# Performance work log

Measured on AMD Instinct MI355X. Metric: run time of the kernel, lower is better.

Reference implementation:

```python
import jax, jax.numpy as jnp
import numpy as np

B, C, H, W = 2, 32, 128, 128
K = 5            # window_size
NH = 2           # num_heads
HD = C // NH     # head_dim = 16
KK = K * K
HID = int(2 * C * 2.0)  # mlp hidden = dim*2*mlp_ratio = 128
SCALE = HD ** -0.5


def _ln(x, w, b, eps=1e-5):
    m = jnp.mean(x, -1, keepdims=True)
    v = jnp.var(x, -1, keepdims=True)
    return (x - m) * jax.lax.rsqrt(v + eps) * w + b


def _windows(t):
    # t: [B,H,W,C] -> [B,H,W,C,K*K]; zero-padded KxK neighborhood per pixel
    # (same layout as nn.Unfold: kernel position is the fastest-varying axis).
    p = (K - 1) // 2
    Hc, Wc = t.shape[1], t.shape[2]
    tp = jnp.pad(t, ((0, 0), (p, p), (p, p), (0, 0)))
    return jnp.stack([tp[:, i:i + Hc, j:j + Wc, :] for i in range(K) for j in range(K)], axis=-1)


def _rel_index():
    # Swin-style relative position index for a KxK window -> [KK,KK] ints
    c = jnp.stack(jnp.meshgrid(jnp.arange(K), jnp.arange(K), indexing='ij'), 0).reshape(2, -1)
    r = (c[:, :, None] - c[:, None, :]).transpose(1, 2, 0) + (K - 1)
    return r[..., 0] * (2 * K - 1) + r[..., 1]


def _ckbd_mask(h, w):
    # checkerboard attention mask: [L, KK, KK] additive (0 or -100)
    ck = jnp.zeros((h, w), jnp.float32)
    ck = ck.at[0::2, 1::2].set(1.0).at[1::2, 0::2].set(1.0)
    cw = _windows(ck[None, :, :, None])[0, :, :, 0, :].reshape(h * w, KK)  # [L,KK]
    m = cw[:, :, None] * cw[:, None, :]
    return jnp.where(m == 1.0, 0.0, -100.0)


def setup_inputs() -> dict:
    key = jax.random.key(0)
    ks = jax.random.split(key, 8)
    p = lambda k, s: (0.02 * jax.random.normal(k, s)).astype(jnp.float32)
    return dict(
        x=jax.random.normal(ks[0], (B, C, H, W), dtype=jnp.float32),
        qkv_w=p(ks[1], (3 * C, C)), qkv_b=jnp.zeros((3 * C,), jnp.float32),
        rel_table=p(ks[2], ((2 * K - 1) ** 2, NH)),
        norm1_w=jnp.ones((C,), jnp.float32), norm1_b=jnp.zeros((C,), jnp.float32),
        norm2_w=jnp.ones((2 * C,), jnp.float32), norm2_b=jnp.zeros((2 * C,), jnp.float32),
        proj_w=p(ks[3], (2 * C, 2 * C)), proj_b=jnp.zeros((2 * C,), jnp.float32),
        fusion_w=p(ks[4], (2 * C, C, K, K)), fusion_b=jnp.zeros((2 * C,), jnp.float32),
        mlp_w1=p(ks[5], (HID, 2 * C)), mlp_b1=jnp.zeros((HID,), jnp.float32),
        mlp_w2=p(ks[6], (2 * C, HID)), mlp_b2=jnp.zeros((2 * C,), jnp.float32),
    )


def reference(x, qkv_w, qkv_b, rel_table, norm1_w, norm1_b, norm2_w, norm2_b,
              proj_w, proj_b, fusion_w, fusion_b, mlp_w1, mlp_b1, mlp_w2, mlp_b2):
    Bs, Cs, Hs, Ws = x.shape
    L = Hs * Ws
    xt = x.reshape(Bs, Cs, L).transpose(0, 2, 1)          # [B,L,C]
    xn = _ln(xt, norm1_w, norm1_b)
    qkv = jnp.einsum('blc,oc->blo', xn, qkv_w) + qkv_b     # [B,L,3C]
    qkv = qkv.reshape(Bs, Hs, Ws, 3, Cs)
    q, k, v = qkv[..., 0, :], qkv[..., 1, :], qkv[..., 2, :]  # each [B,H,W,C]

    def heads(t):
        # windows -> [B,L,C,KK]; split C as (head_dim, num_heads) to match the
        # original reshape(B,L,head_dim,num_heads,KK).permute(0,1,3,4,2)
        w_ = _windows(t).reshape(Bs, L, HD, NH, KK)
        return w_.transpose(0, 1, 3, 4, 2)                 # [B,L,nh,KK,hd]

    qh, kh, vh = heads(q), heads(k), heads(v)
    attn = jnp.einsum('blhqd,blhkd->blhqk', qh * SCALE, kh)  # [B,L,nh,KK,KK]

    bias = rel_table[_rel_index().reshape(-1)].reshape(KK, KK, NH).transpose(2, 0, 1)
    attn = attn + bias[None, None]
    attn = attn + _ckbd_mask(Hs, Ws)[None, :, None]
    attn = jax.nn.softmax(attn, axis=-1)

    o = jnp.einsum('blhqk,blhkd->blhqd', attn, vh)           # [B,L,nh,KK,hd]
    # -> [B,L,K,K,nh,hd] -> [B,L,K,K,C] (head-major channel order, as in torch)
    o = o.reshape(Bs, L, NH, K, K, HD).transpose(0, 1, 3, 4, 2, 5).reshape(Bs, L, K, K, Cs)
    # fusion: Conv2d(C, 2C, kernel=K) on [BL,C,K,K] with no padding == full contraction
    y = jnp.einsum('blijc,ocij->blo', o, fusion_w) + fusion_b  # [B,L,2C]
    y = jnp.einsum('blc,oc->blo', y, proj_w) + proj_b
    h1 = _ln(y, norm2_w, norm2_b)
    mlp = jnp.einsum('blh,oh->blo',
                     jax.nn.gelu(jnp.einsum('blc,hc->blh', h1, mlp_w1) + mlp_b1, approximate=False),
                     mlp_w2) + mlp_b2
    y = y + mlp
    return y.transpose(0, 2, 1).reshape(Bs, 2 * Cs, Hs, Ws)
```

## Files before the change

### kernel.cpp

```cpp
#include <hip/hip_runtime.h>
#include <cstdint>
#include <cstddef>

#define HH 128
#define WW 128
#define LL 16384
#define BL 32768

typedef float  f32x4  __attribute__((ext_vector_type(4)));
typedef __fp16 h2     __attribute__((ext_vector_type(2)));
typedef __fp16 h8     __attribute__((ext_vector_type(8)));

union U32H { unsigned u; h2 h; };

static __device__ __forceinline__ float fdot2(h2 a, h2 b, float c) {
  return __builtin_amdgcn_fdot2(a, b, c, false);
}
static __device__ __forceinline__ unsigned pkh2(float a, float b) {
  h2 h = __builtin_amdgcn_cvt_pkrtz(a, b);
  U32H t; t.h = h; return t.u;
}
static __device__ __forceinline__ h2 bcasth(float a) {
  return __builtin_amdgcn_cvt_pkrtz(a, a);
}
static __device__ __forceinline__ unsigned short f2h(float x) {
  union { __fp16 h; unsigned short u; } c; c.h = (__fp16)x; return c.u;
}

#define LOADH8(dst, ptr) { \
  uint4 _a = *(const uint4*)(ptr); uint4 _b = *(const uint4*)((ptr)+8); U32H _t; \
  _t.u=_a.x; dst[0]=_t.h; _t.u=_a.y; dst[1]=_t.h; _t.u=_a.z; dst[2]=_t.h; _t.u=_a.w; dst[3]=_t.h; \
  _t.u=_b.x; dst[4]=_t.h; _t.u=_b.y; dst[5]=_t.h; _t.u=_b.z; dst[6]=_t.h; _t.u=_b.w; dst[7]=_t.h; }

__global__ __launch_bounds__(256) void k_combine(
    const float* __restrict__ proj_w, const float* __restrict__ proj_b,
    const float* __restrict__ fw, const float* __restrict__ fb,
    const float* __restrict__ w1, const float* __restrict__ w2,
    unsigned short* __restrict__ wctT, float* __restrict__ bc,
    unsigned short* __restrict__ w1h, unsigned short* __restrict__ w2h)
{
  if (blockIdx.x == 200) {
    int o = threadIdx.x;
    if (o < 64) {
      float acc = proj_b[o];
      for (int m = 0; m < 64; ++m) acc = fmaf(proj_w[o*64+m], fb[m], acc);
      bc[o] = acc;
    }
    return;
  }
  if (blockIdx.x == 201) {
    for (int i = threadIdx.x; i < 8192; i += 256) w1h[i] = f2h(w1[i]);
    return;
  }
  if (blockIdx.x == 202) {
    for (int i = threadIdx.x; i < 8192; i += 256) w2h[i] = f2h(w2[i]);
    return;
  }
  int gid = blockIdx.x * 256 + threadIdx.x;
  int o  = gid / 800;
  int kk = gid - o * 800;
  int c  = kk & 31;
  int t  = kk >> 5;
  int in = c * 25 + t;
  float acc = 0.f;
  for (int m = 0; m < 64; ++m) acc = fmaf(proj_w[o*64+m], fw[m*800+in], acc);
  wctT[gid] = f2h(acc);
}

__global__ __launch_bounds__(128) void k_ln_qkv(
    const float* __restrict__ x, const float* __restrict__ qkv_w,
    const float* __restrict__ qkv_b, const float* __restrict__ n1w,
    const float* __restrict__ n1b, unsigned short* __restrict__ qo,
    unsigned short* __restrict__ ko, unsigned short* __restrict__ vo)
{
  __shared__ float sW[32*32];
  __shared__ float sB[32];
  __shared__ float sNw[32], sNb[32];
  int p = blockIdx.y;
  for (int i = threadIdx.x; i < 32*32; i += 128) sW[i] = qkv_w[p*1024 + i];
  if (threadIdx.x < 32) {
    sB[threadIdx.x]  = qkv_b[p*32 + threadIdx.x];
    sNw[threadIdx.x] = n1w[threadIdx.x];
    sNb[threadIdx.x] = n1b[threadIdx.x];
  }
  __syncthreads();
  int gid = blockIdx.x * 128 + threadIdx.x;
  int b = gid >> 14, l = gid & (LL - 1);
  const float* xp = x + (size_t)b * 32 * LL + l;
  float xv[32];
  float mean = 0.f;
  #pragma unroll
  for (int c = 0; c < 32; ++c) { xv[c] = xp[(size_t)c * LL]; mean += xv[c]; }
  mean *= 0.03125f;
  float var = 0.f;
  #pragma unroll
  for (int c = 0; c < 32; ++c) { float d = xv[c] - mean; var = fmaf(d, d, var); }
  float rs = rsqrtf(var * 0.03125f + 1e-5f);
  #pragma unroll
  for (int c = 0; c < 32; ++c) xv[c] = (xv[c] - mean) * rs * sNw[c] + sNb[c];
  float ao[32];
  #pragma unroll
  for (int o = 0; o < 32; ++o) {
    const float* wr = &sW[o * 32];
    float acc = sB[o];
    #pragma unroll
    for (int c = 0; c < 32; ++c) acc = fmaf(xv[c], wr[c], acc);
    ao[(o & 1) * 16 + (o >> 1)] = acc;
  }
  unsigned short* op = (p == 0 ? qo : p == 1 ? ko : vo) + (size_t)gid * 32;
  #pragma unroll
  for (int e = 0; e < 4; ++e) {
    uint4 pk4;
    pk4.x = pkh2(ao[e*8+0], ao[e*8+1]);
    pk4.y = pkh2(ao[e*8+2], ao[e*8+3]);
    pk4.z = pkh2(ao[e*8+4], ao[e*8+5]);
    pk4.w = pkh2(ao[e*8+6], ao[e*8+7]);
    *(uint4*)(op + e*8) = pk4;
  }
}

#define TH 4
#define TW 8
#define NPOS 96
#define KVSTR 24
#define OSTRU 264

__global__ __launch_bounds__(256, 3) void k_attn(
    const unsigned short* __restrict__ qi, const unsigned short* __restrict__ ki,
    const unsigned short* __restrict__ vi, const float* __restrict__ rel_table,
    const unsigned short* __restrict__ wctT, const float* __restrict__ bc,
    float* __restrict__ y2)
{
  __shared__ __align__(16) unsigned short sQ[192*KVSTR];
  __shared__ __align__(16) unsigned short sK[192*KVSTR];
  __shared__ __align__(16) unsigned short sV[192*KVSTR];
  __shared__ __align__(16) unsigned short sO[32*OSTRU];
  __shared__ float sRT[162];
  __shared__ float sPar[NPOS];

  int tid = threadIdx.x;
  int lane = tid & 63, wv = tid >> 6;
  int b  = blockIdx.z;
  int h0 = blockIdx.y * TH, w0 = blockIdx.x * TW;

  for (int i = tid; i < 162; i += 256) sRT[i] = rel_table[i];
  if (tid < NPOS) {
    int ph = tid / 12, pw = tid - ph * 12;
    int h2v = h0 + ph - 2, w2v = w0 + pw - 2;
    bool valid = ((unsigned)h2v < HH) && ((unsigned)w2v < WW);
    sPar[tid] = (valid && (((h2v + w2v) & 1) == 1)) ? 1.f : 0.f;
  }
  for (int idx = tid; idx < 1152; idx += 256) {
    int arr = idx / 384;
    int rem = idx - arr * 384;
    int pos = rem >> 2, q4 = rem & 3;
    int nh = q4 >> 1, half = q4 & 1;
    int ph = pos / 12, pw = pos - ph * 12;
    int h2v = h0 + ph - 2, w2v = w0 + pw - 2;
    uint4 val = make_uint4(0u, 0u, 0u, 0u);
    if (((unsigned)h2v < HH) && ((unsigned)w2v < WW)) {
      const unsigned short* src = (arr == 0 ? ki : arr == 1 ? vi : qi)
                       + ((size_t)((b << 14) + (h2v << 7) + w2v)) * 32 + nh * 16 + half * 8;
      val = *(const uint4*)src;
    }
    unsigned short* dp = (arr == 0 ? sK : arr == 1 ? sV : sQ)
                       + (nh * 96 + pos) * KVSTR + half * 8;
    *(uint4*)dp = val;
  }
  __syncthreads();

  f32x4 acc[2] = {{0.f,0.f,0.f,0.f},{0.f,0.f,0.f,0.f}};
  int ocol = wv * 16 + (lane & 15);

  for (int it = 0; it < 4; ++it) {
    int g = wv * 2 + (lane >> 5);
    int pr = it * 4 + (g >> 1);
    int nh = g & 1;
    int nhb = nh * 96;
    if (pr <= 12) {
      int nrr = (pr < 12) ? 2 : 1;
      int loc = lane & 31;
      int ly = loc >> 3, lx = loc & 7;
      int posb = ly * 12 + lx;
      int tq0 = 2*pr, tq1 = 2*pr + 1;
      int iq0 = tq0/5, jq0 = tq0 - iq0*5;
      int iq1 = tq1/5, jq1 = tq1 - iq1*5;
      int pq0 = posb + iq0*12 + jq0; pq0 = pq0 > 95 ? 95 : pq0;
      int pq1 = posb + iq1*12 + jq1; pq1 = pq1 > 95 ? 95 : pq1;
      float parq0 = sPar[pq0], parq1 = sPar[pq1];
      h2 q0[8], q1[8];
      LOADH8(q0, &sQ[(nhb+pq0)*KVSTR]);
      LOADH8(q1, &sQ[(nhb+pq1)*KVSTR]);
      float s0 = 0.f, s1 = 0.f;
      h2 oo0[8], oo1[8];
      #pragma unroll
      for (int e = 0; e < 8; ++e) { oo0[e] = (h2)(__fp16)0.f; oo1[e] = (h2)(__fp16)0.f; }
      #pragma unroll 1
      for (int ik = 0; ik < 5; ++ik) {
        int rb0 = ((iq0-ik+4)*9 + jq0 + 4)*2 + nh;
        int rb1 = ((iq1-ik+4)*9 + jq1 + 4)*2 + nh;
        #pragma unroll
        for (int jk = 0; jk < 5; ++jk) {
          int pk = posb + ik*12 + jk;
          h2 kh[8];
          LOADH8(kh, &sK[(nhb+pk)*KVSTR]);
          float park = sPar[pk];
          float mk = (park == 1.f) ? 0.f : -100.f;
          float a0 = 0.f, a1 = 0.f;
          #pragma unroll
          for (int u = 0; u < 8; ++u) {
            a0 = fdot2(q0[u], kh[u], a0);
            a1 = fdot2(q1[u], kh[u], a1);
          }
          int i0 = rb0 - 2*jk; i0 = i0 > 161 ? 161 : i0;
          int i1 = rb1 - 2*jk; i1 = i1 > 161 ? 161 : i1;
          float e0 = __expf(fmaf(parq0, mk, fmaf(a0, 0.25f, sRT[i0])));
          float e1 = __expf(fmaf(parq1, mk, fmaf(a1, 0.25f, sRT[i1])));
          s0 += e0; s1 += e1;
          h2 e0h = bcasth(e0), e1h = bcasth(e1);
          h2 vh[8];
          LOADH8(vh, &sV[(nhb+pk)*KVSTR]);
          #pragma unroll
          for (int u = 0; u < 8; ++u) {
            oo0[u] = e0h * vh[u] + oo0[u];
            oo1[u] = e1h * vh[u] + oo1[u];
          }
        }
      }
      #define WRITE_ROW(OO, SS, TQ) { \
        h2 ih = bcasth(1.f / (SS)); \
        int kl = ((TQ) - it*8) * 32 + nh * 16; \
        union { h2 h[8]; uint4 u4[2]; } R; \
        _Pragma("unroll") \
        for (int u = 0; u < 8; ++u) R.h[u] = OO[u] * ih; \
        *(uint4*)&sO[loc*OSTRU + kl] = R.u4[0]; \
        *(uint4*)&sO[loc*OSTRU + kl + 8] = R.u4[1]; }
      WRITE_ROW(oo0, s0, tq0);
      if (1 < nrr) WRITE_ROW(oo1, s1, tq1);
      #undef WRITE_ROW
    }
    __syncthreads();
    int ktn = (it < 3) ? 8 : 1;
    const unsigned short* bcol = wctT + (size_t)ocol * 800 + it * 256 + (lane >> 4) * 8;
    for (int kt = 0; kt < ktn; ++kt) {
      h8 bfrag = *(const h8*)(bcol + kt * 32);
      #pragma unroll
      for (int mt = 0; mt < 2; ++mt) {
        h8 afrag = *(const h8*)&sO[(mt*16 + (lane & 15))*OSTRU + kt*32 + (lane >> 4)*8];
        acc[mt] = __builtin_amdgcn_mfma_f32_16x16x32_f16(afrag, bfrag, acc[mt], 0, 0, 0);
      }
    }
    __syncthreads();
  }
  float bco = bc[ocol];
  #pragma unroll
  for (int mt = 0; mt < 2; ++mt) {
    #pragma unroll
    for (int r2 = 0; r2 < 4; ++r2) {
      int loc = mt * 16 + (lane >> 4) * 4 + r2;
      int ly = loc >> 3, lx = loc & 7;
      int gid = (b << 14) + ((h0 + ly) << 7) + (w0 + lx);
      y2[(size_t)gid * 64 + ocol] = acc[mt][r2] + bco;
    }
  }
}

__global__ __launch_bounds__(256) void k_mlp(
    const float* __restrict__ y2, const float* __restrict__ n2w,
    const float* __restrict__ n2b, const unsigned short* __restrict__ w1h,
    const float* __restrict__ b1, const unsigned short* __restrict__ w2h,
    const float* __restrict__ b2, float* __restrict__ out)
{
  __shared__ __align__(16) unsigned short sA[64*72];
  __shared__ __align__(16) unsigned short sH[64*136];
  int tid = threadIdx.x;
  int lane = tid & 63, wv = tid >> 6;
  int m0 = blockIdx.x * 64;
  {
    int r = tid >> 2, qd = tid & 3;
    const float* yp = y2 + (size_t)(m0 + r) * 64 + qd * 16;
    float xv[16];
    float s = 0.f;
    #pragma unroll
    for (int e = 0; e < 4; ++e) {
      float4 t4 = *(const float4*)(yp + e*4);
      xv[4*e] = t4.x; xv[4*e+1] = t4.y; xv[4*e+2] = t4.z; xv[4*e+3] = t4.w;
      s += t4.x + t4.y + t4.z + t4.w;
    }
    s += __shfl_xor(s, 1);
    s += __shfl_xor(s, 2);
    float mean = s * (1.f/64.f);
    float v = 0.f;
    #pragma unroll
    for (int e = 0; e < 16; ++e) { float d = xv[e] - mean; v = fmaf(d, d, v); }
    v += __shfl_xor(v, 1);
    v += __shfl_xor(v, 2);
    float rs = rsqrtf(v * (1.f/64.f) + 1e-5f);
    #pragma unroll
    for (int u = 0; u < 8; ++u) {
      int c0 = qd*16 + 2*u;
      float h0v = (xv[2*u]   - mean) * rs * n2w[c0]   + n2b[c0];
      float h1v = (xv[2*u+1] - mean) * rs * n2w[c0+1] + n2b[c0+1];
      *(unsigned*)&sA[r*72 + c0] = pkh2(h0v, h1v);
    }
  }
  __syncthreads();
  f32x4 acc1[4][2];
  #pragma unroll
  for (int mt = 0; mt < 4; ++mt)
    #pragma unroll
    for (int nt = 0; nt < 2; ++nt) acc1[mt][nt] = (f32x4){0.f,0.f,0.f,0.f};
  #pragma unroll
  for (int kt = 0; kt < 2; ++kt) {
    #pragma unroll
    for (int nt = 0; nt < 2; ++nt) {
      int ncol = wv*32 + nt*16 + (lane & 15);
      h8 bfrag = *(const h8*)(w1h + ncol*64 + kt*32 + (lane >> 4)*8);
      #pragma unroll
      for (int mt = 0; mt < 4; ++mt) {
        h8 afrag = *(const h8*)&sA[(mt*16 + (lane & 15))*72 + kt*32 + (lane >> 4)*8];
        acc1[mt][nt] = __builtin_amdgcn_mfma_f32_16x16x32_f16(afrag, bfrag, acc1[mt][nt], 0, 0, 0);
      }
    }
  }
  #pragma unroll
  for (int nt = 0; nt < 2; ++nt) {
    int ncol = wv*32 + nt*16 + (lane & 15);
    float b1v = b1[ncol];
    #pragma unroll
    for (int mt = 0; mt < 4; ++mt) {
      #pragma unroll
      for (int r2 = 0; r2 < 4; ++r2) {
        int mrow = mt*16 + (lane >> 4)*4 + r2;
        float h = acc1[mt][nt][r2] + b1v;
        float g = 0.5f * h * (1.f + erff(h * 0.70710678118f));
        sH[mrow*136 + ncol] = f2h(g);
      }
    }
  }
  __syncthreads();
  f32x4 acc2[4];
  #pragma unroll
  for (int mt = 0; mt < 4; ++mt) acc2[mt] = (f32x4){0.f,0.f,0.f,0.f};
  int ocol = wv*16 + (lane & 15);
  #pragma unroll
  for (int kt = 0; kt < 4; ++kt) {
    h8 bfrag = *(const h8*)(w2h + ocol*128 + kt*32 + (lane >> 4)*8);
    #pragma unroll
    for (int mt = 0; mt < 4; ++mt) {
      h8 afrag = *(const h8*)&sH[(mt*16 + (lane & 15))*136 + kt*32 + (lane >> 4)*8];
      acc2[mt] = __builtin_amdgcn_mfma_f32_16x16x32_f16(afrag, bfrag, acc2[mt], 0, 0, 0);
    }
  }
  float b2v = b2[ocol];
  int bb = m0 >> 14;
  #pragma unroll
  for (int mt = 0; mt < 4; ++mt) {
    int mrow = mt*16 + (lane >> 4)*4;
    int l = m0 + mrow;
    const float* yp = y2 + (size_t)l * 64 + ocol;
    float4 o4;
    o4.x = yp[0]   + acc2[mt][0] + b2v;
    o4.y = yp[64]  + acc2[mt][1] + b2v;
    o4.z = yp[128] + acc2[mt][2] + b2v;
    o4.w = yp[192] + acc2[mt][3] + b2v;
    *(float4*)&out[(size_t)bb * 64 * LL + (size_t)ocol * LL + (l - (bb << 14))] = o4;
  }
}

extern "C" void kernel_launch(void* const* d_in, const int* in_sizes, int n_in,
                              void* d_out, int out_size, void* d_ws, size_t ws_size,
                              hipStream_t stream) {
  const float* x         = (const float*)d_in[0];
  const float* qkv_w     = (const float*)d_in[1];
  const float* qkv_b     = (const float*)d_in[2];
  const float* rel_table = (const float*)d_in[3];
  const float* n1w       = (const float*)d_in[4];
  const float* n1b       = (const float*)d_in[5];
  const float* n2w       = (const float*)d_in[6];
  const float* n2b       = (const float*)d_in[7];
  const float* proj_w    = (const float*)d_in[8];
  const float* proj_b    = (const float*)d_in[9];
  const float* fw        = (const float*)d_in[10];
  const float* fb        = (const float*)d_in[11];
  const float* w1        = (const float*)d_in[12];
  const float* b1        = (const float*)d_in[13];
  const float* w2        = (const float*)d_in[14];
  const float* b2        = (const float*)d_in[15];

  char* ws = (char*)d_ws;
  unsigned short* q    = (unsigned short*)(ws);
  unsigned short* k    = (unsigned short*)(ws + 2097152);
  unsigned short* v    = (unsigned short*)(ws + 4194304);
  float*          y2   = (float*)(ws + 6291456);
  unsigned short* wctT = (unsigned short*)(ws + 14680064);
  float*          bc   = (float*)(ws + 14782464);
  unsigned short* w1h  = (unsigned short*)(ws + 14782720);
  unsigned short* w2h  = (unsigned short*)(ws + 14799104);
  float* out = (float*)d_out;

  k_combine<<<203, 256, 0, stream>>>(proj_w, proj_b, fw, fb, w1, w2, wctT, bc, w1h, w2h);
  k_ln_qkv<<<dim3(BL/128, 3), 128, 0, stream>>>(x, qkv_w, qkv_b, n1w, n1b, q, k, v);
  k_attn<<<dim3(WW/TW, HH/TH, 2), 256, 0, stream>>>(q, k, v, rel_table, wctT, bc, y2);
  k_mlp<<<BL/64, 256, 0, stream>>>(y2, n2w, n2b, w1h, b1, w2h, b2, out);
}
```

Before: 95.42 us.

## Shrink attention tile to 2x8 pixels with 16-lane groups and two phases

The attention+fusion kernel now handles a 2x8 pixel tile instead of 4x8. Each 16-lane group processes a query-row pair per head, so the query work runs in two phases instead of four. The fusion GEMM uses a single 16-row MFMA tile over longer K chunks, shared memory per block shrinks, and the occupancy hint rises from 3 to 4. The point is fewer barriers and higher occupancy, at the cost of more halo reloading of K/V/Q per output pixel (72 positions for 16 pixels versus 96 for 32) and reading the fusion weights twice as often overall.

```diff
diff --git a/kernel.cpp b/kernel.cpp
--- a/kernel.cpp
+++ b/kernel.cpp
@@ -119,22 +119,22 @@
   }
 }
 
-#define TH 4
+#define TH 2
 #define TW 8
-#define NPOS 96
-#define KVSTR 24
-#define OSTRU 264
-
-__global__ __launch_bounds__(256, 3) void k_attn(
+#define NPOS 72
+#define KVSTR 26
+#define OSTRU 516
+
+__global__ __launch_bounds__(256, 4) void k_attn(
     const unsigned short* __restrict__ qi, const unsigned short* __restrict__ ki,
     const unsigned short* __restrict__ vi, const float* __restrict__ rel_table,
     const unsigned short* __restrict__ wctT, const float* __restrict__ bc,
     float* __restrict__ y2)
 {
-  __shared__ __align__(16) unsigned short sQ[192*KVSTR];
-  __shared__ __align__(16) unsigned short sK[192*KVSTR];
-  __shared__ __align__(16) unsigned short sV[192*KVSTR];
-  __shared__ __align__(16) unsigned short sO[32*OSTRU];
+  __shared__ __align__(16) unsigned short sQ[144*KVSTR];
+  __shared__ __align__(16) unsigned short sK[144*KVSTR];
+  __shared__ __align__(16) unsigned short sV[144*KVSTR];
+  __shared__ __align__(16) unsigned short sO[16*OSTRU];
   __shared__ float sRT[162];
   __shared__ float sPar[NPOS];
 
@@ -150,9 +150,9 @@
     bool valid = ((unsigned)h2v < HH) && ((unsigned)w2v < WW);
     sPar[tid] = (valid && (((h2v + w2v) & 1) == 1)) ? 1.f : 0.f;
   }
-  for (int idx = tid; idx < 1152; idx += 256) {
-    int arr = idx / 384;
-    int rem = idx - arr * 384;
+  for (int idx = tid; idx < 864; idx += 256) {
+    int arr = idx / 288;
+    int rem = idx - arr * 288;
     int pos = rem >> 2, q4 = rem & 3;
     int nh = q4 >> 1, half = q4 & 1;
     int ph = pos / 12, pw = pos - ph * 12;
@@ -164,29 +164,31 @@
       val = *(const uint4*)src;
     }
     unsigned short* dp = (arr == 0 ? sK : arr == 1 ? sV : sQ)
-                       + (nh * 96 + pos) * KVSTR + half * 8;
+                       + (nh * 72 + pos) * KVSTR + half * 8;
     *(uint4*)dp = val;
   }
   __syncthreads();
 
-  f32x4 acc[2] = {{0.f,0.f,0.f,0.f},{0.f,0.f,0.f,0.f}};
+  f32x4 acc = {0.f, 0.f, 0.f, 0.f};
   int ocol = wv * 16 + (lane & 15);
 
-  for (int it = 0; it < 4; ++it) {
-    int g = wv * 2 + (lane >> 5);
-    int pr = it * 4 + (g >> 1);
-    int nh = g & 1;
-    int nhb = nh * 96;
-    if (pr <= 12) {
-      int nrr = (pr < 12) ? 2 : 1;
-      int loc = lane & 31;
+  for (int it = 0; it < 2; ++it) {
+    int slot = wv * 4 + (lane >> 4);
+    int pr = slot >> 1;
+    int nh = slot & 1;
+    int nhb = nh * 72;
+    int tqb = it * 16;
+    int tq0 = tqb + 2*pr;
+    if (tq0 <= 24) {
+      int nrr = (tq0 + 1 <= 24) ? 2 : 1;
+      int tq1 = tq0 + 1;
+      int loc = lane & 15;
       int ly = loc >> 3, lx = loc & 7;
       int posb = ly * 12 + lx;
-      int tq0 = 2*pr, tq1 = 2*pr + 1;
       int iq0 = tq0/5, jq0 = tq0 - iq0*5;
       int iq1 = tq1/5, jq1 = tq1 - iq1*5;
-      int pq0 = posb + iq0*12 + jq0; pq0 = pq0 > 95 ? 95 : pq0;
-      int pq1 = posb + iq1*12 + jq1; pq1 = pq1 > 95 ? 95 : pq1;
+      int pq0 = posb + iq0*12 + jq0; pq0 = pq0 > 71 ? 71 : pq0;
+      int pq1 = posb + iq1*12 + jq1; pq1 = pq1 > 71 ? 71 : pq1;
       float parq0 = sPar[pq0], parq1 = sPar[pq1];
       h2 q0[8], q1[8];
       LOADH8(q0, &sQ[(nhb+pq0)*KVSTR]);
@@ -229,7 +231,7 @@
       }
       #define WRITE_ROW(OO, SS, TQ) { \
         h2 ih = bcasth(1.f / (SS)); \
-        int kl = ((TQ) - it*8) * 32 + nh * 16; \
+        int kl = ((TQ) - tqb) * 32 + nh * 16; \
         union { h2 h[8]; uint4 u4[2]; } R; \
         _Pragma("unroll") \
         for (int u = 0; u < 8; ++u) R.h[u] = OO[u] * ih; \
@@ -240,28 +242,22 @@
       #undef WRITE_ROW
     }
     __syncthreads();
-    int ktn = (it < 3) ? 8 : 1;
-    const unsigned short* bcol = wctT + (size_t)ocol * 800 + it * 256 + (lane >> 4) * 8;
+    int ktn = it ? 9 : 16;
+    const unsigned short* bcol = wctT + (size_t)ocol * 800 + it * 512 + (lane >> 4) * 8;
     for (int kt = 0; kt < ktn; ++kt) {
       h8 bfrag = *(const h8*)(bcol + kt * 32);
-      #pragma unroll
-      for (int mt = 0; mt < 2; ++mt) {
-        h8 afrag = *(const h8*)&sO[(mt*16 + (lane & 15))*OSTRU + kt*32 + (lane >> 4)*8];
-        acc[mt] = __builtin_amdgcn_mfma_f32_16x16x32_f16(afrag, bfrag, acc[mt], 0, 0, 0);
-      }
+      h8 afrag = *(const h8*)&sO[(lane & 15)*OSTRU + kt*32 + (lane >> 4)*8];
+      acc = __builtin_amdgcn_mfma_f32_16x16x32_f16(afrag, bfrag, acc, 0, 0, 0);
     }
     __syncthreads();
   }
   float bco = bc[ocol];
   #pragma unroll
-  for (int mt = 0; mt < 2; ++mt) {
-    #pragma unroll
-    for (int r2 = 0; r2 < 4; ++r2) {
-      int loc = mt * 16 + (lane >> 4) * 4 + r2;
-      int ly = loc >> 3, lx = loc & 7;
-      int gid = (b << 14) + ((h0 + ly) << 7) + (w0 + lx);
-      y2[(size_t)gid * 64 + ocol] = acc[mt][r2] + bco;
-    }
+  for (int r2 = 0; r2 < 4; ++r2) {
+    int loc = (lane >> 4) * 4 + r2;
+    int ly = loc >> 3, lx = loc & 7;
+    int gid = (b << 14) + ((h0 + ly) << 7) + (w0 + lx);
+    y2[(size_t)gid * 64 + ocol] = acc[r2] + bco;
   }
 }
 
```

Result: slower. 98.67 us (+3.4%).

## Skip checkerboard-masked keys in interior attention blocks via parity-class scheduling

Applied to the files above, without the earlier changes.

Pixels in each attention block are regrouped by checkerboard parity class, so each wavefront handles same-parity queries. In interior blocks (no padding), keys the -100 mask zeros out are skipped statically via templated modes. Query rows with no mask are processed without the mask arithmetic, and boundary blocks keep the full masked path. The fusion GEMM is reorganised into two larger phases with a wider sO buffer, trading more LDS per block and fewer barriers for less exp/FMA work. Skipping the masked keys drops terms of about exp(-100) relative to the unmasked ones, which is a tiny numerical difference.

```diff
diff --git a/kernel.cpp b/kernel.cpp
--- a/kernel.cpp
+++ b/kernel.cpp
@@ -123,7 +123,90 @@
 #define TW 8
 #define NPOS 96
 #define KVSTR 24
-#define OSTRU 264
+#define OSTRU 524
+
+template<int MODE>
+static __device__ __forceinline__ void attn_pair(
+    int tqA, int tqB, int nh, bool wA, bool wB,
+    int posb, int sOrow, int klbase,
+    const unsigned short* __restrict__ sQ, const unsigned short* __restrict__ sK,
+    const unsigned short* __restrict__ sV, unsigned short* __restrict__ sO,
+    const float* __restrict__ sRT, const float* __restrict__ sPar)
+{
+  const int nhb = nh * 96;
+  int iqA = tqA / 5, jqA = tqA - iqA * 5;
+  int iqB = tqB / 5, jqB = tqB - iqB * 5;
+  int pqA = posb + iqA * 12 + jqA;
+  int pqB = posb + iqB * 12 + jqB;
+  float parqA = 0.f, parqB = 0.f;
+  if (MODE == 3) { parqA = sPar[pqA]; parqB = sPar[pqB]; }
+  h2 qA[8], qB[8];
+  LOADH8(qA, &sQ[(nhb + pqA) * KVSTR]);
+  LOADH8(qB, &sQ[(nhb + pqB) * KVSTR]);
+  const int bbA = (iqA * 9 + jqA) * 2 + 80 + nh;
+  const int bbB = (iqB * 9 + jqB) * 2 + 80 + nh;
+  float sA = 0.f, sB = 0.f;
+  h2 ooA[8], ooB[8];
+  #pragma unroll
+  for (int e = 0; e < 8; ++e) { ooA[e] = (h2)(__fp16)0.f; ooB[e] = (h2)(__fp16)0.f; }
+  #pragma unroll 1
+  for (int ik = 0; ik < 5; ++ik) {
+    int pkrow = posb + ik * 12;
+    int bA = bbA - ik * 18, bB = bbB - ik * 18;
+    auto body = [&](int jk) {
+      int pk = pkrow + jk;
+      h2 kh[8];
+      LOADH8(kh, &sK[(nhb + pk) * KVSTR]);
+      float aA = 0.f, aB = 0.f;
+      #pragma unroll
+      for (int u = 0; u < 8; ++u) { aA = fdot2(qA[u], kh[u], aA); aB = fdot2(qB[u], kh[u], aB); }
+      float biasA = sRT[bA - 2 * jk], biasB = sRT[bB - 2 * jk];
+      float eA, eB;
+      if (MODE == 3) {
+        float park = sPar[pk];
+        float mk = (park == 1.f) ? 0.f : -100.f;
+        eA = __expf(fmaf(parqA, mk, fmaf(aA, 0.25f, biasA)));
+        eB = __expf(fmaf(parqB, mk, fmaf(aB, 0.25f, biasB)));
+      } else {
+        eA = __expf(fmaf(aA, 0.25f, biasA));
+        eB = __expf(fmaf(aB, 0.25f, biasB));
+      }
+      sA += eA; sB += eB;
+      h2 eAh = bcasth(eA), eBh = bcasth(eB);
+      h2 vh[8];
+      LOADH8(vh, &sV[(nhb + pk) * KVSTR]);
+      #pragma unroll
+      for (int u = 0; u < 8; ++u) { ooA[u] = eAh * vh[u] + ooA[u]; ooB[u] = eBh * vh[u] + ooB[u]; }
+    };
+    if (MODE == 0 || MODE == 3) {
+      body(0); body(1); body(2); body(3); body(4);
+    } else if (MODE == 1) {
+      if ((ik & 1) == 0) { body(1); body(3); }
+      else { body(0); body(2); body(4); }
+    } else {
+      if ((ik & 1) == 0) { body(0); body(2); body(4); }
+      else { body(1); body(3); }
+    }
+  }
+  if (wA) {
+    h2 ih = bcasth(1.f / sA);
+    int kl = (tqA - klbase) * 32 + nh * 16;
+    union { h2 h[8]; uint4 u4[2]; } R;
+    #pragma unroll
+    for (int u = 0; u < 8; ++u) R.h[u] = ooA[u] * ih;
+    *(uint4*)&sO[sOrow * OSTRU + kl] = R.u4[0];
+    *(uint4*)&sO[sOrow * OSTRU + kl + 8] = R.u4[1];
+  }
+  if (wB) {
+    h2 ih = bcasth(1.f / sB);
+    int kl = (tqB - klbase) * 32 + nh * 16;
+    union { h2 h[8]; uint4 u4[2]; } R;
+    #pragma unroll
+    for (int u = 0; u < 8; ++u) R.h[u] = ooB[u] * ih;
+    *(uint4*)&sO[sOrow * OSTRU + kl] = R.u4[0];
+    *(uint4*)&sO[sOrow * OSTRU + kl + 8] = R.u4[1];
+  }
+}
 
 __global__ __launch_bounds__(256, 3) void k_attn(
     const unsigned short* __restrict__ qi, const unsigned short* __restrict__ ki,
@@ -142,6 +225,7 @@
   int lane = tid & 63, wv = tid >> 6;
   int b  = blockIdx.z;
   int h0 = blockIdx.y * TH, w0 = blockIdx.x * TW;
+  bool fastb = (blockIdx.y >= 1) && (blockIdx.y <= 30) && (blockIdx.x >= 1) && (blockIdx.x <= 14);
 
   for (int i = tid; i < 162; i += 256) sRT[i] = rel_table[i];
   if (tid < NPOS) {
@@ -172,77 +256,31 @@
   f32x4 acc[2] = {{0.f,0.f,0.f,0.f},{0.f,0.f,0.f,0.f}};
   int ocol = wv * 16 + (lane & 15);
 
-  for (int it = 0; it < 4; ++it) {
-    int g = wv * 2 + (lane >> 5);
-    int pr = it * 4 + (g >> 1);
-    int nh = g & 1;
-    int nhb = nh * 96;
-    if (pr <= 12) {
-      int nrr = (pr < 12) ? 2 : 1;
-      int loc = lane & 31;
-      int ly = loc >> 3, lx = loc & 7;
-      int posb = ly * 12 + lx;
-      int tq0 = 2*pr, tq1 = 2*pr + 1;
-      int iq0 = tq0/5, jq0 = tq0 - iq0*5;
-      int iq1 = tq1/5, jq1 = tq1 - iq1*5;
-      int pq0 = posb + iq0*12 + jq0; pq0 = pq0 > 95 ? 95 : pq0;
-      int pq1 = posb + iq1*12 + jq1; pq1 = pq1 > 95 ? 95 : pq1;
-      float parq0 = sPar[pq0], parq1 = sPar[pq1];
-      h2 q0[8], q1[8];
-      LOADH8(q0, &sQ[(nhb+pq0)*KVSTR]);
-      LOADH8(q1, &sQ[(nhb+pq1)*KVSTR]);
-      float s0 = 0.f, s1 = 0.f;
-      h2 oo0[8], oo1[8];
-      #pragma unroll
-      for (int e = 0; e < 8; ++e) { oo0[e] = (h2)(__fp16)0.f; oo1[e] = (h2)(__fp16)0.f; }
-      #pragma unroll 1
-      for (int ik = 0; ik < 5; ++ik) {
-        int rb0 = ((iq0-ik+4)*9 + jq0 + 4)*2 + nh;
-        int rb1 = ((iq1-ik+4)*9 + jq1 + 4)*2 + nh;
-        #pragma unroll
-        for (int jk = 0; jk < 5; ++jk) {
-          int pk = posb + ik*12 + jk;
-          h2 kh[8];
-          LOADH8(kh, &sK[(nhb+pk)*KVSTR]);
-          float park = sPar[pk];
-          float mk = (park == 1.f) ? 0.f : -100.f;
-          float a0 = 0.f, a1 = 0.f;
-          #pragma unroll
-          for (int u = 0; u < 8; ++u) {
-            a0 = fdot2(q0[u], kh[u], a0);
-            a1 = fdot2(q1[u], kh[u], a1);
-          }
-          int i0 = rb0 - 2*jk; i0 = i0 > 161 ? 161 : i0;
-          int i1 = rb1 - 2*jk; i1 = i1 > 161 ? 161 : i1;
-          float e0 = __expf(fmaf(parq0, mk, fmaf(a0, 0.25f, sRT[i0])));
-          float e1 = __expf(fmaf(parq1, mk, fmaf(a1, 0.25f, sRT[i1])));
-          s0 += e0; s1 += e1;
-          h2 e0h = bcasth(e0), e1h = bcasth(e1);
-          h2 vh[8];
-          LOADH8(vh, &sV[(nhb+pk)*KVSTR]);
-          #pragma unroll
-          for (int u = 0; u < 8; ++u) {
-            oo0[u] = e0h * vh[u] + oo0[u];
-            oo1[u] = e1h * vh[u] + oo1[u];
-          }
-        }
-      }
-      #define WRITE_ROW(OO, SS, TQ) { \
-        h2 ih = bcasth(1.f / (SS)); \
-        int kl = ((TQ) - it*8) * 32 + nh * 16; \
-        union { h2 h[8]; uint4 u4[2]; } R; \
-        _Pragma("unroll") \
-        for (int u = 0; u < 8; ++u) R.h[u] = OO[u] * ih; \
-        *(uint4*)&sO[loc*OSTRU + kl] = R.u4[0]; \
-        *(uint4*)&sO[loc*OSTRU + kl + 8] = R.u4[1]; }
-      WRITE_ROW(oo0, s0, tq0);
-      if (1 < nrr) WRITE_ROW(oo1, s1, tq1);
-      #undef WRITE_ROW
-    }
-    __syncthreads();
-    int ktn = (it < 3) ? 8 : 1;
-    const unsigned short* bcol = wctT + (size_t)ocol * 800 + it * 256 + (lane >> 4) * 8;
-    for (int kt = 0; kt < ktn; ++kt) {
+  int cls = wv & 1;
+  int l16 = lane & 15;
+  int nh  = wv >> 1;
+  int kk4 = lane >> 4;
+  int ly  = l16 >> 2;
+  int lx  = 2 * (l16 & 3) + ((cls + ly) & 1);
+  int posb  = ly * 12 + lx;
+  int sOrow = cls * 16 + l16;
+
+  if (fastb) {
+    if (cls == 0) {
+      attn_pair<0>(4*kk4,   4*kk4+2, nh, true, true, posb, sOrow, 0, sQ, sK, sV, sO, sRT, sPar);
+      attn_pair<1>(4*kk4+1, 4*kk4+3, nh, true, true, posb, sOrow, 0, sQ, sK, sV, sO, sRT, sPar);
+    } else {
+      attn_pair<0>(4*kk4+1, 4*kk4+3, nh, true, true, posb, sOrow, 0, sQ, sK, sV, sO, sRT, sPar);
+      attn_pair<2>(4*kk4,   4*kk4+2, nh, true, true, posb, sOrow, 0, sQ, sK, sV, sO, sRT, sPar);
+    }
+  } else {
+    attn_pair<3>(4*kk4,   4*kk4+2, nh, true, true, posb, sOrow, 0, sQ, sK, sV, sO, sRT, sPar);
+    attn_pair<3>(4*kk4+1, 4*kk4+3, nh, true, true, posb, sOrow, 0, sQ, sK, sV, sO, sRT, sPar);
+  }
+  __syncthreads();
+  {
+    const unsigned short* bcol = wctT + (size_t)ocol * 800 + (lane >> 4) * 8;
+    for (int kt = 0; kt < 16; ++kt) {
       h8 bfrag = *(const h8*)(bcol + kt * 32);
       #pragma unroll
       for (int mt = 0; mt < 2; ++mt) {
@@ -250,16 +288,56 @@
         acc[mt] = __builtin_amdgcn_mfma_f32_16x16x32_f16(afrag, bfrag, acc[mt], 0, 0, 0);
       }
     }
-    __syncthreads();
-  }
+  }
+  __syncthreads();
+
+  {
+    int LqA = 16, LqB = 18; bool LwA = false, LwB = false;
+    int SqA = 17, SqB = 19; bool SwA = false, SwB = false;
+    if (cls == 0) {
+      if (kk4 == 0)      { LwA = LwB = true; SwA = SwB = true; }
+      else if (kk4 == 1) { LqA = 20; LqB = 22; LwA = LwB = true; SqA = 21; SqB = 23; SwA = SwB = true; }
+      else if (kk4 == 2) { LqA = 24; LqB = 24; LwA = true; }
+    } else {
+      if (kk4 == 0)      { LqA = 17; LqB = 19; LwA = LwB = true; SqA = 16; SqB = 18; SwA = SwB = true; }
+      else if (kk4 == 1) { LqA = 21; LqB = 23; LwA = LwB = true; SqA = 20; SqB = 22; SwA = SwB = true; }
+      else if (kk4 == 2) { SqA = 24; SqB = 24; SwA = true; }
+    }
+    if (fastb) {
+      if (cls == 0) {
+        attn_pair<0>(LqA, LqB, nh, LwA, LwB, posb, sOrow, 16, sQ, sK, sV, sO, sRT, sPar);
+        attn_pair<1>(SqA, SqB, nh, SwA, SwB, posb, sOrow, 16, sQ, sK, sV, sO, sRT, sPar);
+      } else {
+        attn_pair<0>(LqA, LqB, nh, LwA, LwB, posb, sOrow, 16, sQ, sK, sV, sO, sRT, sPar);
+        attn_pair<2>(SqA, SqB, nh, SwA, SwB, posb, sOrow, 16, sQ, sK, sV, sO, sRT, sPar);
+      }
+    } else {
+      attn_pair<3>(LqA, LqB, nh, LwA, LwB, posb, sOrow, 16, sQ, sK, sV, sO, sRT, sPar);
+      attn_pair<3>(SqA, SqB, nh, SwA, SwB, posb, sOrow, 16, sQ, sK, sV, sO, sRT, sPar);
+    }
+  }
+  __syncthreads();
+  {
+    const unsigned short* bcol = wctT + (size_t)ocol * 800 + 512 + (lane >> 4) * 8;
+    for (int kt = 0; kt < 9; ++kt) {
+      h8 bfrag = *(const h8*)(bcol + kt * 32);
+      #pragma unroll
+      for (int mt = 0; mt < 2; ++mt) {
+        h8 afrag = *(const h8*)&sO[(mt*16 + (lane & 15))*OSTRU + kt*32 + (lane >> 4)*8];
+        acc[mt] = __builtin_amdgcn_mfma_f32_16x16x32_f16(afrag, bfrag, acc[mt], 0, 0, 0);
+      }
+    }
+  }
+  __syncthreads();
+
   float bco = bc[ocol];
   #pragma unroll
   for (int mt = 0; mt < 2; ++mt) {
     #pragma unroll
     for (int r2 = 0; r2 < 4; ++r2) {
-      int loc = mt * 16 + (lane >> 4) * 4 + r2;
-      int ly = loc >> 3, lx = loc & 7;
-      int gid = (b << 14) + ((h0 + ly) << 7) + (w0 + lx);
+      int ly2 = lane >> 4;
+      int lx2 = 2 * r2 + ((mt + ly2) & 1);
+      int gid = (b << 14) + ((h0 + ly2) << 7) + (w0 + lx2);
       y2[(size_t)gid * 64 + ocol] = acc[mt][r2] + bco;
     }
   }
```

Result: faster. 92.80 us (-2.8%).
